# Optimization experiments

Hardware: AMD Instinct MI355X
Metric: run time of the kernel (lower is better)

## Reference

```python
import jax, jax.numpy as jnp
import numpy as np

B, L, D = 4, 2048, 1024
EV = 64            # event_embed_dim
EXPAND = 2
DI = EXPAND * D    # d_inner = 2048
N = 16             # d_state
K = 4              # d_conv
DT_RANK = (D + 15) // 16  # 64
EPS = 1e-5


def setup_inputs() -> dict:
    key = jax.random.key(0)
    ks = jax.random.split(key, 16)
    g = lambda k, shape, s=0.02: (jax.random.normal(k, shape, dtype=jnp.float32) * s)
    return {
        "x": jax.random.normal(ks[0], (B, L, D), dtype=jnp.float32),
        "event_emb": jax.random.normal(ks[1], (B, L, EV), dtype=jnp.float32),
        "W_in": g(ks[2], (D + EV, D)),
        "b_in": jnp.zeros((D,), jnp.float32),
        "ln_g": jnp.ones((D,), jnp.float32),
        "ln_b": jnp.zeros((D,), jnp.float32),
        "in_proj_w": g(ks[3], (D, 2 * DI)),
        "conv_w": g(ks[4], (DI, K), 0.1),
        "conv_b": jnp.zeros((DI,), jnp.float32),
        "x_proj_w": g(ks[5], (DI, DT_RANK + 2 * N)),
        "dt_proj_w": g(ks[6], (DT_RANK, DI), 0.1),
        "dt_proj_b": jnp.full((DI,), -4.6, jnp.float32),  # ~softplus^-1(0.01)
        "A_log": jnp.log(jnp.broadcast_to(jnp.arange(1, N + 1, dtype=jnp.float32), (DI, N))),
        "D_param": jnp.ones((DI,), jnp.float32),
        "out_proj_w": g(ks[7], (DI, D)),
    }


def _mamba_block(x, event_emb, W_in, b_in, ln_g, ln_b, in_proj_w, conv_w, conv_b,
                 x_proj_w, dt_proj_w, dt_proj_b, A_log, D_param, out_proj_w):
    d_conv = conv_w.shape[1]
    n_state = A_log.shape[1]
    dt_rank = dt_proj_w.shape[0]
    Lx = x.shape[1]

    aug = jnp.concatenate([x, event_emb], axis=-1) @ W_in + b_in   # [B,L,D]
    residual = aug
    mu = aug.mean(-1, keepdims=True)
    var = jnp.mean((aug - mu) ** 2, axis=-1, keepdims=True)
    h = (aug - mu) * jax.lax.rsqrt(var + EPS) * ln_g + ln_b

    xz = h @ in_proj_w                                             # [B,L,2*DI]
    xh, z = jnp.split(xz, 2, axis=-1)

    # causal depthwise conv1d (width d_conv)
    xp = jnp.pad(xh, ((0, 0), (d_conv - 1, 0), (0, 0)))
    xc = conv_b
    for k in range(d_conv):
        xc = xc + conv_w[:, k] * xp[:, k:k + Lx, :]
    xc = jax.nn.silu(xc)                                           # [B,L,DI]

    dbl = xc @ x_proj_w                                            # [B,L,dt_rank+2N]
    dt, Bm, Cm = jnp.split(dbl, [dt_rank, dt_rank + n_state], axis=-1)
    dt = jax.nn.softplus(dt @ dt_proj_w + dt_proj_b)               # [B,L,DI]
    A = -jnp.exp(A_log)                                            # [DI,N]

    def step(hst, inp):
        dt_t, B_t, C_t, u_t = inp                                  # [B,DI],[B,N],[B,N],[B,DI]
        dA = jnp.exp(dt_t[:, :, None] * A)                         # [B,DI,N]
        dBu = (dt_t * u_t)[:, :, None] * B_t[:, None, :]           # [B,DI,N]
        hst = dA * hst + dBu
        y_t = jnp.einsum('bdn,bn->bd', hst, C_t)
        return hst, y_t

    h0 = jnp.zeros((xc.shape[0], xc.shape[2], n_state), xc.dtype)
    xs = (dt.transpose(1, 0, 2), Bm.transpose(1, 0, 2),
          Cm.transpose(1, 0, 2), xc.transpose(1, 0, 2))
    _, ys = jax.lax.scan(step, h0, xs)                             # [L,B,DI]
    y = ys.transpose(1, 0, 2) + D_param * xc
    y = y * jax.nn.silu(z)
    return residual + y @ out_proj_w                               # [B,L,D]


def reference(x, event_emb, W_in, b_in, ln_g, ln_b, in_proj_w, conv_w, conv_b,
              x_proj_w, dt_proj_w, dt_proj_b, A_log, D_param, out_proj_w):
    return _mamba_block(x, event_emb, W_in, b_in, ln_g, ln_b, in_proj_w, conv_w,
                        conv_b, x_proj_w, dt_proj_w, dt_proj_b, A_log, D_param,
                        out_proj_w)
```

## Files before the change

kernel.cpp:

```cpp
#include <hip/hip_runtime.h>
#include <cstdint>
#include <cstddef>

#define DEV __device__ __forceinline__

typedef __bf16 bf16x8 __attribute__((ext_vector_type(8)));
typedef float f32x4 __attribute__((ext_vector_type(4)));

DEV unsigned short f2bf(float f) {
  unsigned u = __builtin_bit_cast(unsigned, f);
  u += 0x7fffu + ((u >> 16) & 1u);
  return (unsigned short)(u >> 16);
}
DEV float bf2f(unsigned short h) {
  return __builtin_bit_cast(float, (unsigned)h << 16);
}

__global__ __launch_bounds__(256)
void k_prep(const float* __restrict__ x, const float* __restrict__ ev,
            unsigned short* __restrict__ Aaug,
            const float* __restrict__ W_in, unsigned short* __restrict__ WinT,
            const float* __restrict__ ipW, unsigned short* __restrict__ ipT,
            const float* __restrict__ xpW, unsigned short* __restrict__ xpT,
            const float* __restrict__ dpW, unsigned short* __restrict__ dpT,
            const float* __restrict__ opW, unsigned short* __restrict__ opT) {
  int tid = threadIdx.x;
  int idx = blockIdx.x;
  if (idx < 16384) {
    int col4 = (idx & 1) * 256 + tid;
    if (col4 >= 288) return;
    size_t row = idx >> 1;
    float4 v = make_float4(0.f, 0.f, 0.f, 0.f);
    if (col4 < 256)      v = reinterpret_cast<const float4*>(x + row * 1024)[col4];
    else if (col4 < 272) v = reinterpret_cast<const float4*>(ev + row * 64)[col4 - 256];
    ushort4 o; o.x = f2bf(v.x); o.y = f2bf(v.y); o.z = f2bf(v.z); o.w = f2bf(v.w);
    reinterpret_cast<ushort4*>(Aaug + row * 1152)[col4] = o;
    return;
  }
  idx -= 16384;
  const float* in; unsigned short* out; int R, C, Rout, Cout, gx;
  if (idx < 1152)      { in = W_in; out = WinT; R = 1088; C = 1024; Rout = 1152; Cout = 1024; gx = 32; }
  else if ((idx -= 1152) < 4096) { in = ipW; out = ipT; R = 1024; C = 4096; Rout = 1024; Cout = 4096; gx = 128; }
  else if ((idx -= 4096) < 256)  { in = xpW; out = xpT; R = 2048; C = 96;   Rout = 2048; Cout = 128;  gx = 4;   }
  else if ((idx -= 256) < 128)   { in = dpW; out = dpT; R = 64;   C = 2048; Rout = 64;   Cout = 2048; gx = 64;  }
  else                 { idx -= 128; in = opW; out = opT; R = 2048; C = 1024; Rout = 2048; Cout = 1024; gx = 32; }
  int cx = idx % gx, ry = idx / gx;
  __shared__ float tile[32][33];
  int c0 = cx * 32, r0 = ry * 32;
  int tx = tid & 31, ty = tid >> 5;
#pragma unroll
  for (int i = 0; i < 4; ++i) {
    int r = r0 + ty + i * 8, c = c0 + tx;
    tile[ty + i * 8][tx] = (r < R && c < C) ? in[(size_t)r * C + c] : 0.f;
  }
  __syncthreads();
#pragma unroll
  for (int i = 0; i < 4; ++i) {
    int c = c0 + ty + i * 8, r = r0 + tx;
    if (c < Cout && r < Rout) out[(size_t)c * Rout + r] = f2bf(tile[tx][ty + i * 8]);
  }
}

template <int BN, int EPI>
__global__ __launch_bounds__(512, 1)
void k_gemm8(const unsigned short* __restrict__ A, const unsigned short* __restrict__ Bt,
             int N, int NT, int lda, int ldb,
             float* __restrict__ outF, unsigned short* __restrict__ outB1,
             unsigned short* __restrict__ outB2,
             const float* __restrict__ bias, const unsigned short* __restrict__ residB) {
  static_assert(BN == 128 || BN == 256, "");
  constexpr int NF = BN / 64;
  constexpr int NHF = NF / 2;
  constexpr int BLOADS = BN / 128;
  constexpr int ATILE = 256 * 64;
  constexpr int BTILE = BN * 64;
  constexpr int BUFSZ = ATILE + BTILE;
  __shared__ unsigned short lds[2 * BUFSZ];

  const int tid = threadIdx.x;
  const int lane = tid & 63, w = tid >> 6;
  const int wm = w >> 2, wn = w & 3;
  const int frow = lane & 15, fk = lane >> 4;

  const int nbx = gridDim.x;
  const int nwg = nbx * gridDim.y;
  const int orig = blockIdx.y * nbx + blockIdx.x;
  const int swz = (orig & 7) * (nwg >> 3) + (orig >> 3);
  const int brow = swz / nbx, bcol = swz % nbx;
  const size_t row0 = (size_t)brow * 256, col0 = (size_t)bcol * BN;

  f32x4 acc[8][NF];
#pragma unroll
  for (int i = 0; i < 8; ++i)
#pragma unroll
    for (int j = 0; j < NF; ++j) acc[i][j] = f32x4{0.f, 0.f, 0.f, 0.f};

  bf16x8 afr[4][2], bq0[NHF][2], bq1[NHF][2];

  const int srow = tid >> 3;
  const int g8 = ((tid & 7) ^ (srow & 7)) * 8;
  const size_t offA_h0l0 = (row0 + 0 * 128 + 0 * 64 + srow) * (size_t)lda + g8;
  const size_t offA_h0l1 = (row0 + 1 * 128 + 0 * 64 + srow) * (size_t)lda + g8;
  const size_t offA_h1l0 = (row0 + 0 * 128 + 1 * 64 + srow) * (size_t)lda + g8;
  const size_t offA_h1l1 = (row0 + 1 * 128 + 1 * 64 + srow) * (size_t)lda + g8;
  const size_t offB_h0l0 = (col0 + 0 * (BN / 2) + 0 * 64 + srow) * (size_t)ldb + g8;
  const size_t offB_h1l0 = (col0 + 1 * (BN / 2) + 0 * 64 + srow) * (size_t)ldb + g8;
  const size_t offB_h0l1 = (BLOADS == 2) ? ((col0 + 0 * (BN / 2) + 1 * 64 + srow) * (size_t)ldb + g8) : 0;
  const size_t offB_h1l1 = (BLOADS == 2) ? ((col0 + 1 * (BN / 2) + 1 * 64 + srow) * (size_t)ldb + g8) : 0;

  char* ldsb = reinterpret_cast<char*>(lds);
  const int fr7 = frow & 7;
  const int slot0 = (fk ^ fr7) * 16;
  const int slot1 = ((4 + fk) ^ fr7) * 16;
  const int abase0 = (wm * 128 + frow) * 128 + slot0;
  const int abase1 = (wm * 128 + frow) * 128 + slot1;
  const int bbase0 = (wn * (BN / 4) + frow) * 128 + slot0 + ATILE * 2;
  const int bbase1 = (wn * (BN / 4) + frow) * 128 + slot1 + ATILE * 2;

  auto stageA = [&](int p, int tau, int half) {
    const size_t kadd = (size_t)tau * 64;
    const unsigned short* s0 = A + (half ? offA_h1l0 : offA_h0l0) + kadd;
    const unsigned short* s1 = A + (half ? offA_h1l1 : offA_h0l1) + kadd;
    unsigned short* dst = lds + p * BUFSZ + half * 4096 + w * 512;
    __builtin_amdgcn_global_load_lds(s0, dst, 16, 0, 0);
    __builtin_amdgcn_global_load_lds(s1, dst + 8192, 16, 0, 0);
  };
  auto stageB = [&](int p, int tau, int half) {
    const size_t kadd = (size_t)tau * 64;
    unsigned short* dst = lds + p * BUFSZ + ATILE + half * (BTILE / 2) + w * 512;
    const unsigned short* s0 = Bt + (half ? offB_h1l0 : offB_h0l0) + kadd;
    __builtin_amdgcn_global_load_lds(s0, dst, 16, 0, 0);
    if constexpr (BLOADS == 2) {
      const unsigned short* s1 = Bt + (half ? offB_h1l1 : offB_h0l1) + kadd;
      __builtin_amdgcn_global_load_lds(s1, dst + 4096, 16, 0, 0);
    }
  };
  auto ldA = [&](int p, int mh) {
    const int pb = p * (BUFSZ * 2);
#pragma unroll
    for (int mi = 0; mi < 4; ++mi) {
      const int off = pb + (mh * 64 + mi * 16) * 128;
      afr[mi][0] = *reinterpret_cast<const bf16x8*>(ldsb + abase0 + off);
      afr[mi][1] = *reinterpret_cast<const bf16x8*>(ldsb + abase1 + off);
    }
  };
  auto ldB = [&](int p, int nh, bf16x8 (&bq)[NHF][2]) {
    const int pb = p * (BUFSZ * 2);
#pragma unroll
    for (int ni = 0; ni < NHF; ++ni) {
      const int off = pb + (nh * (BN / 8) + ni * 16) * 128;
      bq[ni][0] = *reinterpret_cast<const bf16x8*>(ldsb + bbase0 + off);
      bq[ni][1] = *reinterpret_cast<const bf16x8*>(ldsb + bbase1 + off);
    }
  };

#define MMAQ(MH, NH, BQ)                                                          \
  do {                                                                            \
    _Pragma("unroll") for (int mi = 0; mi < 4; ++mi)                              \
        _Pragma("unroll") for (int ni = 0; ni < NHF; ++ni)                        \
            _Pragma("unroll") for (int kb = 0; kb < 2; ++kb)                      \
                acc[(MH)*4 + mi][(NH)*NHF + ni] =                                 \
                    __builtin_amdgcn_mfma_f32_16x16x32_bf16(                      \
                        afr[mi][kb], BQ[ni][kb], acc[(MH)*4 + mi][(NH)*NHF + ni], \
                        0, 0, 0);                                                 \
  } while (0)

#define PRIO1 __builtin_amdgcn_s_setprio(1)
#define PRIO0 __builtin_amdgcn_s_setprio(0)
#define BARC  __builtin_amdgcn_s_barrier()
#define SBAR  __builtin_amdgcn_sched_barrier(0)
#define VMCNT_WAIT                                                     \
  do {                                                                 \
    if constexpr (BN == 256)                                           \
      asm volatile("s_waitcnt vmcnt(6)" ::: "memory");                 \
    else                                                               \
      asm volatile("s_waitcnt vmcnt(4)" ::: "memory");                 \
  } while (0)

  stageA(0, 0, 0); stageB(0, 0, 0); stageB(0, 0, 1); stageA(0, 0, 1);
  SBAR;
  stageA(1, 1, 0); stageB(1, 1, 0); stageB(1, 1, 1);
  VMCNT_WAIT;
  BARC; SBAR;

  const int niter = NT >> 1;
  for (int it = 0; it < niter; ++it) {
    int t = 2 * it;
    int t1s = t + 1;
    int t2s = (t + 2 < NT) ? t + 2 : NT - 1;
    int t3s = (t + 3 < NT) ? t + 3 : NT - 1;
    ldA(0, 0); ldB(0, 0, bq0); ldB(0, 1, bq1);
    stageA(1, t1s, 1);
    BARC; PRIO1; MMAQ(0, 0, bq0); MMAQ(0, 1, bq1); PRIO0; BARC;
    ldA(0, 1);
    stageA(0, t2s, 0); stageB(0, t2s, 0); stageB(0, t2s, 1);
    VMCNT_WAIT;
    BARC; PRIO1; MMAQ(1, 1, bq1); MMAQ(1, 0, bq0); PRIO0; BARC;
    ldA(1, 0); ldB(1, 0, bq0); ldB(1, 1, bq1);
    stageA(0, t2s, 1);
    BARC; PRIO1; MMAQ(0, 0, bq0); MMAQ(0, 1, bq1); PRIO0; BARC;
    ldA(1, 1);
    stageA(1, t3s, 0); stageB(1, t3s, 0); stageB(1, t3s, 1);
    VMCNT_WAIT;
    BARC; PRIO1; MMAQ(1, 1, bq1); MMAQ(1, 0, bq0); PRIO0; BARC;
  }

#pragma unroll
  for (int q = 0; q < 8; ++q) {
#pragma unroll
    for (int j = 0; j < NF; ++j) {
#pragma unroll
      for (int r = 0; r < 4; ++r) {
        size_t row = row0 + wm * 128 + q * 16 + fk * 4 + r;
        size_t col = col0 + wn * (BN / 4) + j * 16 + frow;
        float v = acc[q][j][r];
        if constexpr (EPI == 0) {
          outB1[row * N + col] = f2bf(v + bias[col]);
        } else if constexpr (EPI == 1) {
          int hn = N >> 1;
          if ((int)col < hn) outB1[row * hn + col] = f2bf(v);
          else               outB2[row * hn + (col - hn)] = f2bf(v);
        } else {
          outF[row * N + col] = bf2f(residB[row * N + col]) + v;
        }
      }
    }
  }
#undef MMAQ
#undef PRIO1
#undef PRIO0
#undef BARC
#undef SBAR
#undef VMCNT_WAIT
}

template <int EPI>
__global__ __launch_bounds__(256)
void k_gemm(const unsigned short* __restrict__ A, const unsigned short* __restrict__ Bt,
            int N, int K, int lda, int ldb,
            unsigned short* __restrict__ outB1, const float* __restrict__ bias,
            float* __restrict__ outF) {
  __shared__ alignas(16) unsigned short sA[128 * 64];
  __shared__ alignas(16) unsigned short sB[128 * 64];
  int tid = threadIdx.x;
  int lane = tid & 63, w = tid >> 6;
  int nbx = gridDim.x;
  int nwg = nbx * gridDim.y;
  int orig = blockIdx.y * nbx + blockIdx.x;
  int swz = (orig & 7) * (nwg >> 3) + (orig >> 3);
  int brow = swz / nbx, bcol = swz % nbx;
  size_t row0 = (size_t)brow * 128, col0 = (size_t)bcol * 128;
  int ks = 0;
  if constexpr (EPI == 6) { ks = bcol; col0 = 0; }
  const size_t kbase = (size_t)ks * 1024;

  int lrow_s = tid >> 3;
  int g_s = tid & 7;
  int wrow = (w >> 1) * 64, wcol = (w & 1) * 64;
  int frow = lane & 15, fk = lane >> 4;
  f32x4 acc[4][4] = {};

  for (int kt = 0; kt < K; kt += 64) {
    __syncthreads();
#pragma unroll
    for (int r = 0; r < 4; ++r) {
      int lr = r * 32 + lrow_s;
      int gs = g_s ^ (lr & 7);
      const unsigned short* srcA = A + (size_t)(row0 + lr) * lda + kbase + kt + gs * 8;
      const unsigned short* srcB = Bt + (size_t)(col0 + lr) * ldb + kbase + kt + gs * 8;
      unsigned short* dstA = sA + (r * 32 + w * 8) * 64;
      unsigned short* dstB = sB + (r * 32 + w * 8) * 64;
      __builtin_amdgcn_global_load_lds(srcA, dstA, 16, 0, 0);
      __builtin_amdgcn_global_load_lds(srcB, dstB, 16, 0, 0);
    }
    __syncthreads();
#pragma unroll
    for (int kw = 0; kw < 2; ++kw) {
      bf16x8 af[4], bfr[4];
      int gk = kw * 4 + fk;
#pragma unroll
      for (int mi = 0; mi < 4; ++mi) {
        int rr = wrow + mi * 16 + frow;
        af[mi] = *reinterpret_cast<const bf16x8*>(sA + rr * 64 + ((gk ^ (rr & 7)) * 8));
      }
#pragma unroll
      for (int ni = 0; ni < 4; ++ni) {
        int rr = wcol + ni * 16 + frow;
        bfr[ni] = *reinterpret_cast<const bf16x8*>(sB + rr * 64 + ((gk ^ (rr & 7)) * 8));
      }
#pragma unroll
      for (int mi = 0; mi < 4; ++mi)
#pragma unroll
        for (int ni = 0; ni < 4; ++ni)
          acc[mi][ni] = __builtin_amdgcn_mfma_f32_16x16x32_bf16(af[mi], bfr[ni], acc[mi][ni], 0, 0, 0);
    }
  }

#pragma unroll
  for (int mi = 0; mi < 4; ++mi) {
#pragma unroll
    for (int ni = 0; ni < 4; ++ni) {
#pragma unroll
      for (int r = 0; r < 4; ++r) {
        size_t row = row0 + wrow + mi * 16 + fk * 4 + r;
        size_t col = col0 + wcol + ni * 16 + frow;
        float v = acc[mi][ni][r];
        if constexpr (EPI == 6) {
          outF[(size_t)ks * (8192ull * 128) + row * 128 + col] = v;
        } else {
          float xx = v + bias[col];
          float sp = (xx > 15.f) ? xx : __logf(1.f + __expf(xx));
          outB1[row * N + col] = f2bf(sp);
        }
      }
    }
  }
}

__global__ __launch_bounds__(256)
void k_comb(const float* __restrict__ P, unsigned short* __restrict__ dbl) {
  size_t i4 = (size_t)blockIdx.x * 256 + threadIdx.x;
  float4 a = reinterpret_cast<const float4*>(P)[i4];
  float4 b = reinterpret_cast<const float4*>(P + 8192ull * 128)[i4];
  ushort4 o;
  o.x = f2bf(a.x + b.x); o.y = f2bf(a.y + b.y);
  o.z = f2bf(a.z + b.z); o.w = f2bf(a.w + b.w);
  reinterpret_cast<ushort4*>(dbl)[i4] = o;
}

__global__ __launch_bounds__(256)
void k_ln(const unsigned short* __restrict__ aug, const float* __restrict__ gam,
          const float* __restrict__ bet, unsigned short* __restrict__ h) {
  int tid = threadIdx.x;
  size_t row = blockIdx.x;
  ushort4 raw = reinterpret_cast<const ushort4*>(aug + row * 1024)[tid];
  float v0 = bf2f(raw.x), v1 = bf2f(raw.y), v2 = bf2f(raw.z), v3 = bf2f(raw.w);
  float s = v0 + v1 + v2 + v3;
  float ss = v0 * v0 + v1 * v1 + v2 * v2 + v3 * v3;
#pragma unroll
  for (int m = 32; m >= 1; m >>= 1) {
    s += __shfl_xor(s, m, 64);
    ss += __shfl_xor(ss, m, 64);
  }
  __shared__ float rb[8];
  if ((tid & 63) == 0) { rb[tid >> 6] = s; rb[4 + (tid >> 6)] = ss; }
  __syncthreads();
  float ts = rb[0] + rb[1] + rb[2] + rb[3];
  float tss = rb[4] + rb[5] + rb[6] + rb[7];
  float mu = ts * (1.f / 1024.f);
  float var = tss * (1.f / 1024.f) - mu * mu;
  float rs = rsqrtf(var + 1e-5f);
  float4 gv = reinterpret_cast<const float4*>(gam)[tid];
  float4 bv = reinterpret_cast<const float4*>(bet)[tid];
  ushort4 o;
  o.x = f2bf((v0 - mu) * rs * gv.x + bv.x);
  o.y = f2bf((v1 - mu) * rs * gv.y + bv.y);
  o.z = f2bf((v2 - mu) * rs * gv.z + bv.z);
  o.w = f2bf((v3 - mu) * rs * gv.w + bv.w);
  reinterpret_cast<ushort4*>(h + row * 1024)[tid] = o;
}

__global__ __launch_bounds__(256)
void k_conv(const unsigned short* __restrict__ xh, const float* __restrict__ cw,
            const float* __restrict__ cb, unsigned short* __restrict__ xc) {
  size_t row = blockIdx.x;
  int t = (int)(row & 2047);
  size_t rowb = row - t;
  int d = threadIdx.x * 8;
  float acc[8];
  {
    float4 c0 = *reinterpret_cast<const float4*>(cb + d);
    float4 c1 = *reinterpret_cast<const float4*>(cb + d + 4);
    acc[0] = c0.x; acc[1] = c0.y; acc[2] = c0.z; acc[3] = c0.w;
    acc[4] = c1.x; acc[5] = c1.y; acc[6] = c1.z; acc[7] = c1.w;
  }
  float wv[8][4];
#pragma unroll
  for (int j = 0; j < 8; ++j) {
    float4 cj = *reinterpret_cast<const float4*>(cw + (size_t)(d + j) * 4);
    wv[j][0] = cj.x; wv[j][1] = cj.y; wv[j][2] = cj.z; wv[j][3] = cj.w;
  }
#pragma unroll
  for (int k = 0; k < 4; ++k) {
    int tt = t - 3 + k;
    if (tt >= 0) {
      ushort4 va = reinterpret_cast<const ushort4*>(xh + (rowb + tt) * 2048 + d)[0];
      ushort4 vb = reinterpret_cast<const ushort4*>(xh + (rowb + tt) * 2048 + d)[1];
      unsigned short e[8] = {va.x, va.y, va.z, va.w, vb.x, vb.y, vb.z, vb.w};
#pragma unroll
      for (int j = 0; j < 8; ++j) acc[j] += wv[j][k] * bf2f(e[j]);
    }
  }
  ushort4 o0, o1;
#pragma unroll
  for (int j = 0; j < 8; ++j) {
    float sg = 1.f / (1.f + __expf(-acc[j]));
    unsigned short r = f2bf(acc[j] * sg);
    if (j < 4) (&o0.x)[j] = r; else (&o1.x)[j - 4] = r;
  }
  reinterpret_cast<ushort4*>(xc + row * 2048 + d)[0] = o0;
  reinterpret_cast<ushort4*>(xc + row * 2048 + d)[1] = o1;
}

template <bool FINAL>
__global__ __launch_bounds__(256)
void k_scan(const unsigned short* __restrict__ dt, const unsigned short* __restrict__ xc,
            const unsigned short* __restrict__ dbl, const float* __restrict__ A_log,
            float* __restrict__ S, float* __restrict__ SD,
            const float* __restrict__ Hin, const float* __restrict__ Dp,
            const unsigned short* __restrict__ z, unsigned short* __restrict__ yg) {
  int d = blockIdx.x * 256 + threadIdx.x;
  int b = blockIdx.y, c = blockIdx.z;
  int t0 = c * 32;
  size_t hoff = (((size_t)c * 4 + b) * 2048 + d) * 16;
  float An[16], h[16];
  bool fast = true;
#pragma unroll
  for (int n = 0; n < 16; ++n) {
    An[n] = -__expf(A_log[((size_t)d << 4) + n]);
    fast = fast && (__builtin_fabsf(An[n] + (float)(n + 1)) < 1e-4f);
    h[n] = FINAL ? Hin[hoff + n] : 0.f;
  }
  float Dv = FINAL ? Dp[d] : 0.f;
  float dts = 0.f;
  __shared__ float sBC[32][32];
  if (threadIdx.x < 128) {
    int s = threadIdx.x >> 2, j8 = (threadIdx.x & 3) * 8;
    size_t rowg = (size_t)b * 2048 + t0 + s;
    uint4 raw = *reinterpret_cast<const uint4*>(dbl + rowg * 128 + 64 + j8);
    unsigned rr4[4] = {raw.x, raw.y, raw.z, raw.w};
#pragma unroll
    for (int q = 0; q < 4; ++q) {
      sBC[s][j8 + 2 * q]     = bf2f((unsigned short)(rr4[q] & 0xffffu));
      sBC[s][j8 + 2 * q + 1] = bf2f((unsigned short)(rr4[q] >> 16));
    }
  }
  __syncthreads();

  const size_t rbase = ((size_t)b * 2048 + t0) * 2048 + d;
  if (fast) {
    float dtv = bf2f(dt[rbase]);
    float uv  = bf2f(xc[rbase]);
    float zv  = FINAL ? bf2f(z[rbase]) : 0.f;
    for (int si = 0; si < 32; ++si) {
      size_t rnext = rbase + (size_t)(si + 1 < 32 ? si + 1 : 31) * 2048;
      float dtv_n = bf2f(dt[rnext]);
      float uv_n  = bf2f(xc[rnext]);
      float zv_n  = FINAL ? bf2f(z[rnext]) : 0.f;
      float dtu = dtv * uv;
      float y = 0.f;
      if constexpr (!FINAL) dts += dtv;
      float e1 = __expf(-dtv);
      float e2 = e1 * e1;
      float e3 = e2 * e1, e4 = e2 * e2;
      float e8 = e4 * e4, e12 = e8 * e4;
      float base[4] = {e1, e2, e3, e4};
      float mul[4] = {1.f, e4, e8, e12};
#pragma unroll
      for (int n = 0; n < 16; ++n) {
        float a = base[n & 3] * mul[n >> 2];
        h[n] = a * h[n] + dtu * sBC[si][n];
        if constexpr (FINAL) y += h[n] * sBC[si][16 + n];
      }
      if constexpr (FINAL) {
        float sig = 1.f / (1.f + __expf(-zv));
        yg[rbase + (size_t)si * 2048] = f2bf((y + Dv * uv) * (zv * sig));
      }
      dtv = dtv_n; uv = uv_n; zv = zv_n;
    }
  } else {
    for (int si = 0; si < 32; ++si) {
      size_t rr = rbase + (size_t)si * 2048;
      float dtv = bf2f(dt[rr]);
      float uv = bf2f(xc[rr]);
      float dtu = dtv * uv;
      float y = 0.f;
      if constexpr (!FINAL) dts += dtv;
#pragma unroll
      for (int n = 0; n < 16; ++n) {
        float a = __expf(dtv * An[n]);
        h[n] = a * h[n] + dtu * sBC[si][n];
        if constexpr (FINAL) y += h[n] * sBC[si][16 + n];
      }
      if constexpr (FINAL) {
        float zv = bf2f(z[rr]);
        float sig = 1.f / (1.f + __expf(-zv));
        yg[rr] = f2bf((y + Dv * uv) * (zv * sig));
      }
    }
  }
  if constexpr (!FINAL) {
#pragma unroll
    for (int n = 0; n < 16; ++n) S[hoff + n] = h[n];
    SD[((size_t)c * 4 + b) * 2048 + d] = dts;
  }
}

__global__ __launch_bounds__(256)
void k_scanB(float* __restrict__ S, const float* __restrict__ SD,
             const float* __restrict__ A_log) {
  int id = blockIdx.x * 256 + threadIdx.x;
  int n = id & 15, d = (id >> 4) & 2047, b = id >> 15;
  float An = -__expf(A_log[((size_t)d << 4) + n]);
  float h = 0.f;
  for (int c = 0; c < 64; ++c) {
    size_t sdo = ((size_t)c * 4 + b) * 2048 + d;
    size_t o = sdo * 16 + n;
    float s = S[o];
    float p = __expf(An * SD[sdo]);
    S[o] = h;
    h = s + p * h;
  }
}

extern "C" void kernel_launch(void* const* d_in, const int* in_sizes, int n_in,
                              void* d_out, int out_size, void* d_ws, size_t ws_size,
                              hipStream_t stream) {
  const float* x       = (const float*)d_in[0];
  const float* ev      = (const float*)d_in[1];
  const float* W_in    = (const float*)d_in[2];
  const float* b_in    = (const float*)d_in[3];
  const float* ln_g    = (const float*)d_in[4];
  const float* ln_b    = (const float*)d_in[5];
  const float* in_proj = (const float*)d_in[6];
  const float* conv_w  = (const float*)d_in[7];
  const float* conv_b  = (const float*)d_in[8];
  const float* x_proj  = (const float*)d_in[9];
  const float* dt_proj = (const float*)d_in[10];
  const float* dt_b    = (const float*)d_in[11];
  const float* A_log   = (const float*)d_in[12];
  const float* D_par   = (const float*)d_in[13];
  const float* out_w   = (const float*)d_in[14];
  float* out = (float*)d_out;

  char* ws = (char*)d_ws;
  size_t off = 0;
  auto alloc = [&](size_t bytes) {
    char* p = ws + off;
    off = (off + bytes + 255) & ~(size_t)255;
    return p;
  };
  unsigned short* augb  = (unsigned short*)alloc(8192ull * 1024 * 2);
  unsigned short* dtfb  = (unsigned short*)alloc(8192ull * 2048 * 2);
  unsigned short* Aaug  = (unsigned short*)alloc(8192ull * 1152 * 2);
  unsigned short* WinT  = (unsigned short*)alloc(1024ull * 1152 * 2);
  unsigned short* ipT   = (unsigned short*)alloc(4096ull * 1024 * 2);
  unsigned short* xpT   = (unsigned short*)alloc(128ull * 2048 * 2);
  unsigned short* dpT   = (unsigned short*)alloc(2048ull * 64 * 2);
  unsigned short* opT   = (unsigned short*)alloc(1024ull * 2048 * 2);
  unsigned short* xh    = (unsigned short*)alloc(8192ull * 2048 * 2);
  unsigned short* zb    = (unsigned short*)alloc(8192ull * 2048 * 2);
  unsigned short* xcb   = (unsigned short*)alloc(8192ull * 2048 * 2);
  unsigned short* dbl   = (unsigned short*)alloc(8192ull * 128 * 2);
  float* Pd = (float*)alloc(2ull * 8192 * 128 * 4);
  float* Sb = (float*)alloc(64ull * 4 * 2048 * 16 * 4);
  float* SD = (float*)alloc(64ull * 4 * 2048 * 4);
  unsigned short* hb = Aaug;
  unsigned short* yg = xh;

  k_prep<<<dim3(24064), 256, 0, stream>>>(x, ev, Aaug, W_in, WinT, in_proj, ipT,
                                          x_proj, xpT, dt_proj, dpT, out_w, opT);

  k_gemm8<128, 0><<<dim3(8, 32), 512, 0, stream>>>(Aaug, WinT, 1024, 18, 1152, 1152,
                                                   nullptr, augb, nullptr, b_in, nullptr);
  k_ln<<<dim3(8192), 256, 0, stream>>>(augb, ln_g, ln_b, hb);
  k_gemm8<256, 1><<<dim3(16, 32), 512, 0, stream>>>(hb, ipT, 4096, 16, 1024, 1024,
                                                    nullptr, xh, zb, nullptr, nullptr);
  k_conv<<<dim3(8192), 256, 0, stream>>>(xh, conv_w, conv_b, xcb);
  k_gemm<6><<<dim3(2, 64), 256, 0, stream>>>(xcb, xpT, 128, 1024, 2048, 2048,
                                             nullptr, nullptr, Pd);
  k_comb<<<dim3(1024), 256, 0, stream>>>(Pd, dbl);
  k_gemm<3><<<dim3(16, 64), 256, 0, stream>>>(dbl, dpT, 2048, 64, 128, 64,
                                              dtfb, dt_b, nullptr);
  k_scan<false><<<dim3(8, 4, 64), 256, 0, stream>>>(dtfb, xcb, dbl, A_log, Sb, SD,
                                                    nullptr, nullptr, nullptr, nullptr);
  k_scanB<<<dim3(512), 256, 0, stream>>>(Sb, SD, A_log);
  k_scan<true><<<dim3(8, 4, 64), 256, 0, stream>>>(dtfb, xcb, dbl, A_log, nullptr, nullptr,
                                                   Sb, D_par, zb, yg);
  k_gemm8<128, 4><<<dim3(8, 32), 512, 0, stream>>>(yg, opT, 1024, 32, 2048, 2048,
                                                   out, nullptr, nullptr, nullptr, augb);
}
```

Measured before the change: 373.2 us.

## Use double-buffered 128x128 tile GEMM for in_proj instead of 256-wide 8-wave kernel

Adds a new 256-thread GEMM kernel with 128x128 tiles, double-buffered LDS staging via global_load_lds, and XOR-swizzled shared memory. It replaces the 512-thread, 256-wide-tile kernel for the in_proj matmul (8192x4096x1024) that splits its output into xh and z. Smaller tiles produce 2048 workgroups rather than 512, aiming for better occupancy and load balance across CUs. The cost is lower data reuse per tile and more global traffic.

```diff
diff --git a/kernel.cpp b/kernel.cpp
--- a/kernel.cpp
+++ b/kernel.cpp
@@ -232,6 +232,100 @@
 #undef BARC
 #undef SBAR
 #undef VMCNT_WAIT
+}
+
+template <int EPI>
+__global__ __launch_bounds__(256)
+void k_gemm2(const unsigned short* __restrict__ A, const unsigned short* __restrict__ Bt,
+             int N, int K, int lda, int ldb,
+             unsigned short* __restrict__ outB1, unsigned short* __restrict__ outB2) {
+  __shared__ alignas(16) unsigned short sA[2][128 * 64];
+  __shared__ alignas(16) unsigned short sB[2][128 * 64];
+  const int tid = threadIdx.x;
+  const int lane = tid & 63, w = tid >> 6;
+  const int nbx = gridDim.x;
+  const int nwg = nbx * gridDim.y;
+  const int orig = blockIdx.y * nbx + blockIdx.x;
+  const int swz = (orig & 7) * (nwg >> 3) + (orig >> 3);
+  const int brow = swz / nbx, bcol = swz % nbx;
+  const size_t row0 = (size_t)brow * 128, col0 = (size_t)bcol * 128;
+
+  const int lrow_s = tid >> 3;
+  const int g_s = tid & 7;
+  const int wrow = (w >> 1) * 64, wcol = (w & 1) * 64;
+  const int frow = lane & 15, fk = lane >> 4;
+  f32x4 acc[4][4] = {};
+
+  auto stage = [&](int p, int kt) {
+#pragma unroll
+    for (int r = 0; r < 4; ++r) {
+      int lr = r * 32 + lrow_s;
+      int gs = g_s ^ (lr & 7);
+      const unsigned short* srcA = A + (size_t)(row0 + lr) * lda + kt + gs * 8;
+      const unsigned short* srcB = Bt + (size_t)(col0 + lr) * ldb + kt + gs * 8;
+      unsigned short* dstA = sA[p] + (r * 32 + w * 8) * 64;
+      unsigned short* dstB = sB[p] + (r * 32 + w * 8) * 64;
+      __builtin_amdgcn_global_load_lds(srcA, dstA, 16, 0, 0);
+      __builtin_amdgcn_global_load_lds(srcB, dstB, 16, 0, 0);
+    }
+  };
+
+  const int NT = K >> 6;
+  stage(0, 0);
+  asm volatile("s_waitcnt vmcnt(0)" ::: "memory");
+  __builtin_amdgcn_s_barrier();
+  __builtin_amdgcn_sched_barrier(0);
+
+  for (int t = 0; t < NT; ++t) {
+    const int cur = t & 1, nxt = cur ^ 1;
+    const bool more = (t + 1 < NT);
+    if (more) stage(nxt, (t + 1) * 64);
+    __builtin_amdgcn_s_setprio(1);
+#pragma unroll
+    for (int kw = 0; kw < 2; ++kw) {
+      bf16x8 af[4], bfr[4];
+      int gk = kw * 4 + fk;
+#pragma unroll
+      for (int mi = 0; mi < 4; ++mi) {
+        int rr = wrow + mi * 16 + frow;
+        af[mi] = *reinterpret_cast<const bf16x8*>(sA[cur] + rr * 64 + ((gk ^ (rr & 7)) * 8));
+      }
+#pragma unroll
+      for (int ni = 0; ni < 4; ++ni) {
+        int rr = wcol + ni * 16 + frow;
+        bfr[ni] = *reinterpret_cast<const bf16x8*>(sB[cur] + rr * 64 + ((gk ^ (rr & 7)) * 8));
+      }
+#pragma unroll
+      for (int mi = 0; mi < 4; ++mi)
+#pragma unroll
+        for (int ni = 0; ni < 4; ++ni)
+          acc[mi][ni] = __builtin_amdgcn_mfma_f32_16x16x32_bf16(af[mi], bfr[ni], acc[mi][ni], 0, 0, 0);
+    }
+    __builtin_amdgcn_s_setprio(0);
+    if (more) {
+      asm volatile("s_waitcnt vmcnt(0)" ::: "memory");
+      __builtin_amdgcn_s_barrier();
+      __builtin_amdgcn_sched_barrier(0);
+    }
+  }
+
+#pragma unroll
+  for (int mi = 0; mi < 4; ++mi) {
+#pragma unroll
+    for (int ni = 0; ni < 4; ++ni) {
+#pragma unroll
+      for (int r = 0; r < 4; ++r) {
+        size_t row = row0 + wrow + mi * 16 + fk * 4 + r;
+        size_t col = col0 + wcol + ni * 16 + frow;
+        float v = acc[mi][ni][r];
+        if constexpr (EPI == 1) {
+          int hn = N >> 1;
+          if ((int)col < hn) outB1[row * hn + col] = f2bf(v);
+          else               outB2[row * hn + (col - hn)] = f2bf(v);
+        }
+      }
+    }
+  }
 }
 
 template <int EPI>
@@ -564,8 +658,7 @@
   k_gemm8<128, 0><<<dim3(8, 32), 512, 0, stream>>>(Aaug, WinT, 1024, 18, 1152, 1152,
                                                    nullptr, augb, nullptr, b_in, nullptr);
   k_ln<<<dim3(8192), 256, 0, stream>>>(augb, ln_g, ln_b, hb);
-  k_gemm8<256, 1><<<dim3(16, 32), 512, 0, stream>>>(hb, ipT, 4096, 16, 1024, 1024,
-                                                    nullptr, xh, zb, nullptr, nullptr);
+  k_gemm2<1><<<dim3(32, 64), 256, 0, stream>>>(hb, ipT, 4096, 1024, 1024, 1024, xh, zb);
   k_conv<<<dim3(8192), 256, 0, stream>>>(xh, conv_w, conv_b, xcb);
   k_gemm<6><<<dim3(2, 64), 256, 0, stream>>>(xcb, xpT, 128, 1024, 2048, 2048,
                                              nullptr, nullptr, Pd);
```

Measured after the change: 385.6 us. +3.3%, slower.
